# Performance work log

Hardware: AMD Instinct MI355X
Metric: run time of the kernel (lower is better)

The kernel has to match this reference:

```python
import jax, jax.numpy as jnp
import numpy as np

EPS = 1e-12  # matches F.normalize default eps


def l2norm(x):
    n = jnp.sqrt(jnp.sum(x * x, axis=-1, keepdims=True))
    return x / jnp.maximum(n, EPS)


def setup_inputs() -> dict:
    key = jax.random.key(0)
    ks = jax.random.split(key, 14)
    B, Q, T, V = 128, 128, 64, 196
    Dv, Dt, E = 768, 768, 512
    s = 0.02  # kaiming-ish scale
    inp = {
        "visual_cls": jax.random.normal(ks[0], (Q, Dv), jnp.float32),
        "textual_cls": jax.random.normal(ks[1], (B, Dt), jnp.float32),
        "visual_tokens": jax.random.normal(ks[2], (Q, V, Dv), jnp.float32),
        "textual_tokens": jax.random.normal(ks[3], (B, T, Dt), jnp.float32),
        # linear params (torch nn.Linear convention: y = x @ W.T + b)
        "Wv_cls": jax.random.normal(ks[4], (E, Dv), jnp.float32) * s,
        "bv_cls": jnp.zeros((E,), jnp.float32),
        "Wt_cls": jax.random.normal(ks[5], (E, Dt), jnp.float32) * s,
        "bt_cls": jnp.zeros((E,), jnp.float32),
        "Wv_tok": jax.random.normal(ks[6], (E, Dv), jnp.float32) * s,
        "bv_tok": jnp.zeros((E,), jnp.float32),
        "Wt_tok": jax.random.normal(ks[7], (E, Dt), jnp.float32) * s,
        "bt_tok": jnp.zeros((E,), jnp.float32),
        "text_length": jax.random.randint(ks[8], (B,), 1, T + 1, jnp.int64),
    }
    return inp


def reference(visual_cls, textual_cls, visual_tokens, textual_tokens,
              Wv_cls, bv_cls, Wt_cls, bt_cls,
              Wv_tok, bv_tok, Wt_tok, bt_tok, text_length):
    # cls projections
    visual_embed_cls = visual_cls @ Wv_cls.T + bv_cls      # [Q, E]
    textual_embed_cls = textual_cls @ Wt_cls.T + bt_cls    # [B, E]
    # token projections + l2 norm
    ve = l2norm(visual_tokens @ Wv_tok.T + bv_tok)          # [Q, V, E]
    te = l2norm(textual_tokens @ Wt_tok.T + bt_tok)         # [B, T, E]

    B, T, _ = te.shape
    # text mask (built but NOT used in sim, faithful to original)
    text_mask = (jnp.arange(T)[None, :] < text_length[:, None]).astype(jnp.float32)

    # ColBERT-style MaxSim: [B, Q, T, V]
    logits = jnp.einsum('btd,qvd->bqtv', te, ve)
    Vdim = logits.shape[-1]
    Tdim = logits.shape[-2]
    t2v = jnp.sum(jnp.max(logits, axis=-1), axis=2) / Vdim  # [B, Q]
    v2t = jnp.sum(jnp.max(logits, axis=-2), axis=2) / Tdim  # [B, Q]
    text_to_image_sim = 0.5 * (t2v + v2t)                    # [B, Q]

    return (visual_embed_cls, textual_embed_cls, ve, te, text_mask,
            text_to_image_sim)
```

## Files before the change

kernel.cpp:

```cpp
#include <hip/hip_runtime.h>
#include <hip/hip_bf16.h>

typedef __bf16 bf16_t;
typedef __bf16 bf16x8 __attribute__((ext_vector_type(8)));
typedef __bf16 bf16x4 __attribute__((ext_vector_type(4)));
typedef float f32x4 __attribute__((ext_vector_type(4)));
typedef float f32x16 __attribute__((ext_vector_type(16)));

#define MFMA16(a, b, c) __builtin_amdgcn_mfma_f32_16x16x32_bf16((a), (b), (c), 0, 0, 0)
#define MFMA32(a, b, c) __builtin_amdgcn_mfma_f32_32x32x16_bf16((a), (b), (c), 0, 0, 0)

#define WN 393216
#define VP_ELEMS 14680064ULL
#define TP_ELEMS 4194304ULL

__device__ inline bf16x8 cvt8(const float* __restrict__ p) {
    f32x4 a = *reinterpret_cast<const f32x4*>(p);
    f32x4 b = *reinterpret_cast<const f32x4*>(p + 4);
    bf16x8 r;
    r[0] = (bf16_t)a[0]; r[1] = (bf16_t)a[1]; r[2] = (bf16_t)a[2]; r[3] = (bf16_t)a[3];
    r[4] = (bf16_t)b[0]; r[5] = (bf16_t)b[1]; r[6] = (bf16_t)b[2]; r[7] = (bf16_t)b[3];
    return r;
}

__device__ __forceinline__ void gload_lds16(const bf16_t* g, bf16_t* l) {
    __builtin_amdgcn_global_load_lds(
        (const __attribute__((address_space(1))) void*)g,
        (__attribute__((address_space(3))) void*)l, 16, 0, 0);
}

__global__ __launch_bounds__(256) void cvt_w4(
    const float* __restrict__ s0, const float* __restrict__ s1,
    const float* __restrict__ s2, const float* __restrict__ s3,
    bf16_t* __restrict__ d)
{
    int i = blockIdx.x * 256 + threadIdx.x;
    int seg = i / (WN / 4);
    int off = i - seg * (WN / 4);
    const float* s = (seg == 0) ? s0 : (seg == 1) ? s1 : (seg == 2) ? s2 : s3;
    f32x4 v = reinterpret_cast<const f32x4*>(s)[off];
    bf16x4 r;
    r[0] = (bf16_t)v[0]; r[1] = (bf16_t)v[1];
    r[2] = (bf16_t)v[2]; r[3] = (bf16_t)v[3];
    reinterpret_cast<bf16x4*>(d)[i] = r;
}

__global__ __launch_bounds__(256) void zero_tail(bf16_t* __restrict__ vp)
{
    int i = blockIdx.x * 256 + threadIdx.x;
    int off = (i & 63) * 8;
    int ks  = (i >> 6) & 3;
    int c   = (i >> 8) & 7;
    int q   = i >> 11;
    size_t addr = ((size_t)q * 224 + c * 28 + 24 + ks) * 512 + off;
    *reinterpret_cast<f32x4*>(vp + addr) = (f32x4){0.f, 0.f, 0.f, 0.f};
}

template<int PACKED>
__global__ __launch_bounds__(256) void proj_all(
    const float* __restrict__ vtok, const float* __restrict__ ttok,
    const float* __restrict__ vcls, const float* __restrict__ tcls,
    const bf16_t* __restrict__ w_all,
    const float* __restrict__ bvc, const float* __restrict__ btc,
    const float* __restrict__ bvt, const float* __restrict__ btt,
    float* __restrict__ out_base,
    bf16_t* __restrict__ bve, bf16_t* __restrict__ bte)
{
    const int tid  = threadIdx.x;
    const int wave = tid >> 6;
    const int lane = tid & 63;
    const int l16  = lane & 15;
    const int quad = lane >> 4;
    const int e0   = wave * 128;
    const int id   = blockIdx.x;

    const float* A; const bf16_t* W; const float* bias;
    float* out; bf16_t* outb; int seg, m0;
    if (id < 784)       { seg = 0; A = vtok; W = w_all + 2 * WN; bias = bvt;
                          out = out_base + 131072;   outb = bve; m0 = id * 32; }
    else if (id < 1040) { seg = 1; A = ttok; W = w_all + 3 * WN; bias = btt;
                          out = out_base + 12976128; outb = bte; m0 = (id - 784) * 32; }
    else if (id < 1044) { seg = 2; A = vcls; W = w_all;          bias = bvc;
                          out = out_base;             outb = nullptr; m0 = (id - 1040) * 32; }
    else                { seg = 3; A = tcls; W = w_all + WN;     bias = btc;
                          out = out_base + 65536;     outb = nullptr; m0 = (id - 1044) * 32; }

    f32x4 acc[2][8];
#pragma unroll
    for (int rt = 0; rt < 2; ++rt)
#pragma unroll
        for (int t = 0; t < 8; ++t) acc[rt][t] = (f32x4){0.f, 0.f, 0.f, 0.f};

    const float* ar0 = A + (size_t)(m0 + l16) * 768 + quad * 8;
    const float* ar1 = ar0 + (size_t)16 * 768;

    for (int k0 = 0; k0 < 768; k0 += 32) {
        bf16x8 a0 = cvt8(ar0 + k0);
        bf16x8 a1 = cvt8(ar1 + k0);
#pragma unroll
        for (int t = 0; t < 8; ++t) {
            bf16x8 wv = *reinterpret_cast<const bf16x8*>(
                W + (size_t)(e0 + t * 16 + l16) * 768 + quad * 8 + k0);
            acc[0][t] = MFMA16(a0, wv, acc[0][t]);
            acc[1][t] = MFMA16(a1, wv, acc[1][t]);
        }
    }

#pragma unroll
    for (int t = 0; t < 8; ++t) {
        float bv = bias[e0 + t * 16 + l16];
#pragma unroll
        for (int rt = 0; rt < 2; ++rt)
#pragma unroll
            for (int r = 0; r < 4; ++r) acc[rt][t][r] += bv;
    }

    float inv[2][4];
#pragma unroll
    for (int rt = 0; rt < 2; ++rt)
#pragma unroll
        for (int r = 0; r < 4; ++r) inv[rt][r] = 1.f;

    __shared__ float sq[4][32];
    if (seg <= 1) {
#pragma unroll
        for (int rt = 0; rt < 2; ++rt)
#pragma unroll
            for (int r = 0; r < 4; ++r) {
                float s = 0.f;
#pragma unroll
                for (int t = 0; t < 8; ++t) s += acc[rt][t][r] * acc[rt][t][r];
                s += __shfl_xor(s, 1);
                s += __shfl_xor(s, 2);
                s += __shfl_xor(s, 4);
                s += __shfl_xor(s, 8);
                if (l16 == 0) sq[wave][rt * 16 + quad * 4 + r] = s;
            }
        __syncthreads();
#pragma unroll
        for (int rt = 0; rt < 2; ++rt)
#pragma unroll
            for (int r = 0; r < 4; ++r) {
                int row = rt * 16 + quad * 4 + r;
                float tot = sq[0][row] + sq[1][row] + sq[2][row] + sq[3][row];
                inv[rt][r] = 1.0f / fmaxf(sqrtf(tot), 1e-12f);
            }
    }

#pragma unroll
    for (int rt = 0; rt < 2; ++rt)
#pragma unroll
        for (int r = 0; r < 4; ++r) {
            const int   R  = m0 + rt * 16 + quad * 4 + r;
            const float is = inv[rt][r];
            const size_t lin = (size_t)R * 512 + e0 + l16;
#pragma unroll
            for (int t = 0; t < 8; ++t)
                out[lin + t * 16] = acc[rt][t][r] * is;

            if (seg <= 1) {
                if (!PACKED) {
#pragma unroll
                    for (int t = 0; t < 8; ++t)
                        outb[lin + t * 16] = (bf16_t)(acc[rt][t][r] * is);
                } else {
                    size_t fb0; int elem, stride_c;
                    if (seg == 0) {
                        int qq = R / 196, vv = R - qq * 196;
                        fb0  = (size_t)qq * 224 + (vv >> 5) * 4;
                        elem = (((l16 >> 3) * 32 + (vv & 31)) << 3) | (l16 & 7);
                        stride_c = 28;
                    } else {
                        int bb = R >> 6;
                        fb0  = (size_t)bb * 64 + ((R >> 5) & 1) * 4;
                        elem = (((l16 >> 3) * 32 + (R & 31)) << 3) | (l16 & 7);
                        stride_c = 8;
                    }
#pragma unroll
                    for (int t = 0; t < 8; ++t) {
                        int c  = wave * 2 + (t >> 2);
                        int ks = t & 3;
                        outb[(fb0 + (size_t)c * stride_c + ks) * 512 + elem] =
                            (bf16_t)(acc[rt][t][r] * is);
                    }
                }
            }
        }
}

__global__ __launch_bounds__(256) void maxsim32p(
    const bf16_t* __restrict__ tp,
    const bf16_t* __restrict__ vp,
    float* __restrict__ sim)
{
    const int tid  = threadIdx.x;
    const int wave = tid >> 6;
    const int lane = tid & 63;
    const int l32  = lane & 31;
    const int h    = lane >> 5;
    const int bhat = wave >> 1;
    const int tt   = wave & 1;

    const int n  = blockIdx.x;
    const int q  = n >> 6;
    const int bp = n & 63;
    const int b  = bp * 2 + bhat;

    __shared__ bf16_t vs[2][14336];
    __shared__ float  tmax_s[2][64];
    __shared__ float  vmax_s[2][2][224];

    f32x16 acc[7];
#pragma unroll
    for (int vt = 0; vt < 7; ++vt)
#pragma unroll
        for (int r = 0; r < 16; ++r) acc[vt][r] = 0.f;

    const bf16_t* vq = vp + (size_t)q * 114688;
    const bf16_t* tb = tp + (size_t)b * 32768;

    auto issue = [&](int buf, int c) {
        const bf16_t* src = vq + (size_t)c * 14336 + wave * 512 + lane * 8;
        bf16_t* dst = &vs[buf][wave * 512];
#pragma unroll
        for (int g = 0; g < 7; ++g)
            gload_lds16(src + g * 2048, dst + g * 2048);
    };

    issue(0, 0);
#pragma unroll
    for (int c = 0; c < 8; ++c) {
        __syncthreads();
        if (c < 7) issue((c + 1) & 1, c + 1);
        bf16x8 a[4];
        const bf16_t* ta = tb + (size_t)(c * 8 + tt * 4) * 512 + lane * 8;
#pragma unroll
        for (int ks = 0; ks < 4; ++ks)
            a[ks] = *reinterpret_cast<const bf16x8*>(ta + ks * 512);
        const bf16_t* bbase = &vs[c & 1][lane * 8];
#pragma unroll
        for (int ks = 0; ks < 4; ++ks)
#pragma unroll
            for (int vt = 0; vt < 7; ++vt) {
                bf16x8 bv = *reinterpret_cast<const bf16x8*>(
                    bbase + (vt * 4 + ks) * 512);
                acc[vt] = MFMA32(a[ks], bv, acc[vt]);
            }
    }

#pragma unroll
    for (int reg = 0; reg < 16; ++reg) {
        float m = acc[0][reg];
#pragma unroll
        for (int vt = 1; vt < 6; ++vt) m = fmaxf(m, acc[vt][reg]);
        if (l32 < 4) m = fmaxf(m, acc[6][reg]);
        m = fmaxf(m, __shfl_xor(m, 1));
        m = fmaxf(m, __shfl_xor(m, 2));
        m = fmaxf(m, __shfl_xor(m, 4));
        m = fmaxf(m, __shfl_xor(m, 8));
        m = fmaxf(m, __shfl_xor(m, 16));
        if (l32 == 0) {
            int row = tt * 32 + (reg & 3) + 8 * (reg >> 2) + 4 * h;
            tmax_s[bhat][row] = m;
        }
    }
#pragma unroll
    for (int vt = 0; vt < 7; ++vt) {
        float m = acc[vt][0];
#pragma unroll
        for (int reg = 1; reg < 16; ++reg) m = fmaxf(m, acc[vt][reg]);
        m = fmaxf(m, __shfl_xor(m, 32));
        if (h == 0) vmax_s[bhat][tt][vt * 32 + l32] = m;
    }
    __syncthreads();

    if (wave == 0) {
        float t0 = tmax_s[0][lane];
        float t1 = tmax_s[1][lane];
        float c0 = 0.f, c1 = 0.f;
        for (int v = lane; v < 196; v += 64) {
            c0 += fmaxf(vmax_s[0][0][v], vmax_s[0][1][v]);
            c1 += fmaxf(vmax_s[1][0][v], vmax_s[1][1][v]);
        }
#pragma unroll
        for (int mk = 1; mk <= 32; mk <<= 1) {
            t0 += __shfl_xor(t0, mk);
            t1 += __shfl_xor(t1, mk);
            c0 += __shfl_xor(c0, mk);
            c1 += __shfl_xor(c1, mk);
        }
        if (lane == 0) {
            sim[(size_t)(bp * 2 + 0) * 128 + q] = 0.5f * (t0 * (1.0f / 196.0f) + c0 * (1.0f / 64.0f));
            sim[(size_t)(bp * 2 + 1) * 128 + q] = 0.5f * (t1 * (1.0f / 196.0f) + c1 * (1.0f / 64.0f));
        }
    }
}

__global__ __launch_bounds__(256) void maxsim32(
    const bf16_t* __restrict__ te,
    const bf16_t* __restrict__ ve,
    float* __restrict__ sim)
{
    const int tid  = threadIdx.x;
    const int wave = tid >> 6;
    const int lane = tid & 63;
    const int l32  = lane & 31;
    const int h    = lane >> 5;
    const int bhat = wave >> 1;
    const int tt   = wave & 1;

    const int n  = blockIdx.x;
    const int q  = n >> 6;
    const int bp = n & 63;
    const int b  = bp * 2 + bhat;

    __shared__ bf16_t vs[2][224 * 64];
    __shared__ float  tmax_s[2][64];
    __shared__ float  vmax_s[2][2][224];

    f32x16 acc[7];
#pragma unroll
    for (int vt = 0; vt < 7; ++vt)
#pragma unroll
        for (int r = 0; r < 16; ++r) acc[vt][r] = 0.f;

    auto issue = [&](int buf, int c) {
        for (int g = wave; g < 28; g += 4) {
            int r   = g * 8 + (lane >> 3);
            int sr  = r < 196 ? r : 195;
            int seg = (lane & 7) ^ (lane >> 3);
            gload_lds16(ve + ((size_t)q * 196 + sr) * 512 + c * 64 + seg * 8,
                        &vs[buf][g * 512]);
        }
    };

    const size_t tbase = ((size_t)b * 64 + tt * 32 + l32) * 512;

    issue(0, 0);
#pragma unroll
    for (int c = 0; c < 8; ++c) {
        __syncthreads();
        if (c < 7) issue((c + 1) & 1, c + 1);
        bf16x8 a[4];
#pragma unroll
        for (int ks = 0; ks < 4; ++ks)
            a[ks] = *reinterpret_cast<const bf16x8*>(
                te + tbase + c * 64 + ks * 16 + h * 8);
        const int buf = c & 1;
#pragma unroll
        for (int ks = 0; ks < 4; ++ks)
#pragma unroll
            for (int vt = 0; vt < 7; ++vt) {
                int row  = vt * 32 + l32;
                int phys = (ks * 2 + h) ^ (row & 7);
                bf16x8 bv = *reinterpret_cast<const bf16x8*>(
                    &vs[buf][row * 64 + phys * 8]);
                acc[vt] = MFMA32(a[ks], bv, acc[vt]);
            }
    }

#pragma unroll
    for (int reg = 0; reg < 16; ++reg) {
        float m = acc[0][reg];
#pragma unroll
        for (int vt = 1; vt < 6; ++vt) m = fmaxf(m, acc[vt][reg]);
        if (l32 < 4) m = fmaxf(m, acc[6][reg]);
        m = fmaxf(m, __shfl_xor(m, 1));
        m = fmaxf(m, __shfl_xor(m, 2));
        m = fmaxf(m, __shfl_xor(m, 4));
        m = fmaxf(m, __shfl_xor(m, 8));
        m = fmaxf(m, __shfl_xor(m, 16));
        if (l32 == 0) {
            int row = tt * 32 + (reg & 3) + 8 * (reg >> 2) + 4 * h;
            tmax_s[bhat][row] = m;
        }
    }
#pragma unroll
    for (int vt = 0; vt < 7; ++vt) {
        float m = acc[vt][0];
#pragma unroll
        for (int reg = 1; reg < 16; ++reg) m = fmaxf(m, acc[vt][reg]);
        m = fmaxf(m, __shfl_xor(m, 32));
        if (h == 0) vmax_s[bhat][tt][vt * 32 + l32] = m;
    }
    __syncthreads();

    if (wave == 0) {
        float t0 = tmax_s[0][lane];
        float t1 = tmax_s[1][lane];
        float c0 = 0.f, c1 = 0.f;
        for (int v = lane; v < 196; v += 64) {
            c0 += fmaxf(vmax_s[0][0][v], vmax_s[0][1][v]);
            c1 += fmaxf(vmax_s[1][0][v], vmax_s[1][1][v]);
        }
#pragma unroll
        for (int mk = 1; mk <= 32; mk <<= 1) {
            t0 += __shfl_xor(t0, mk);
            t1 += __shfl_xor(t1, mk);
            c0 += __shfl_xor(c0, mk);
            c1 += __shfl_xor(c1, mk);
        }
        if (lane == 0) {
            sim[(size_t)(bp * 2 + 0) * 128 + q] = 0.5f * (t0 * (1.0f / 196.0f) + c0 * (1.0f / 64.0f));
            sim[(size_t)(bp * 2 + 1) * 128 + q] = 0.5f * (t1 * (1.0f / 196.0f) + c1 * (1.0f / 64.0f));
        }
    }
}

__global__ __launch_bounds__(256) void proj_fb(
    const float* __restrict__ A, const float* __restrict__ Wf,
    const float* __restrict__ bias, float* __restrict__ out, int do_l2)
{
    const int tid  = threadIdx.x;
    const int wave = tid >> 6;
    const int lane = tid & 63;
    const int l16  = lane & 15;
    const int quad = lane >> 4;
    const int m0   = blockIdx.x * 16;
    const int e0   = wave * 128;

    f32x4 acc[8];
#pragma unroll
    for (int t = 0; t < 8; ++t) acc[t] = (f32x4){0.f, 0.f, 0.f, 0.f};
    const float* arow = A + (size_t)(m0 + l16) * 768 + quad * 8;
    for (int k0 = 0; k0 < 768; k0 += 32) {
        bf16x8 af = cvt8(arow + k0);
#pragma unroll
        for (int t = 0; t < 8; ++t) {
            bf16x8 wv = cvt8(Wf + (size_t)(e0 + t * 16 + l16) * 768 + quad * 8 + k0);
            acc[t] = MFMA16(af, wv, acc[t]);
        }
    }
#pragma unroll
    for (int t = 0; t < 8; ++t) {
        float bv = bias[e0 + t * 16 + l16];
#pragma unroll
        for (int r = 0; r < 4; ++r) acc[t][r] += bv;
    }
    float inv[4] = {1.f, 1.f, 1.f, 1.f};
    __shared__ float sq[4][16];
    if (do_l2) {
#pragma unroll
        for (int r = 0; r < 4; ++r) {
            float s = 0.f;
#pragma unroll
            for (int t = 0; t < 8; ++t) s += acc[t][r] * acc[t][r];
            s += __shfl_xor(s, 1); s += __shfl_xor(s, 2);
            s += __shfl_xor(s, 4); s += __shfl_xor(s, 8);
            if (l16 == 0) sq[wave][quad * 4 + r] = s;
        }
        __syncthreads();
#pragma unroll
        for (int r = 0; r < 4; ++r) {
            float tot = sq[0][quad * 4 + r] + sq[1][quad * 4 + r]
                      + sq[2][quad * 4 + r] + sq[3][quad * 4 + r];
            inv[r] = 1.0f / fmaxf(sqrtf(tot), 1e-12f);
        }
    }
#pragma unroll
    for (int t = 0; t < 8; ++t)
#pragma unroll
        for (int r = 0; r < 4; ++r)
            out[(size_t)(m0 + quad * 4 + r) * 512 + (e0 + t * 16 + l16)] =
                acc[t][r] * inv[r];
}

__global__ __launch_bounds__(256) void maxsim_fb(
    const float* __restrict__ te, const float* __restrict__ ve,
    float* __restrict__ sim)
{
    const int tid  = threadIdx.x;
    const int wave = tid >> 6;
    const int lane = tid & 63;
    const int l16  = lane & 15;
    const int quad = lane >> 4;
    const int q    = blockIdx.x >> 6;
    const int bp   = blockIdx.x & 63;

    __shared__ bf16_t vsl[208 * 72];
    __shared__ float  maxt_s[2][4][208];
    __shared__ float  t2v_part[2][4];

    f32x4 acc0[13], acc1[13];
#pragma unroll
    for (int vt = 0; vt < 13; ++vt) {
        acc0[vt] = (f32x4){0.f, 0.f, 0.f, 0.f};
        acc1[vt] = (f32x4){0.f, 0.f, 0.f, 0.f};
    }
    const size_t toff0 = ((size_t)(bp * 2) * 64 + wave * 16 + l16) * 512 + quad * 8;
    const size_t toff1 = toff0 + (size_t)64 * 512;

    for (int k0 = 0; k0 < 512; k0 += 64) {
        __syncthreads();
        for (int s = tid; s < 416; s += 256) {
            const int row  = s >> 1;
            const int half = s & 1;
            const int vsrc = row < 196 ? row : 195;
            bf16x8 tmp[4];
            const size_t goff = ((size_t)q * 196 + vsrc) * 512 + k0 + half * 32;
#pragma unroll
            for (int j = 0; j < 4; ++j) tmp[j] = cvt8(ve + goff + j * 8);
            bf16_t* dst = &vsl[row * 72 + half * 32];
#pragma unroll
            for (int j = 0; j < 4; ++j)
                *reinterpret_cast<bf16x8*>(dst + j * 8) = tmp[j];
        }
        __syncthreads();
#pragma unroll
        for (int ks = 0; ks < 2; ++ks) {
            bf16x8 a0 = cvt8(te + toff0 + k0 + ks * 32);
            bf16x8 a1 = cvt8(te + toff1 + k0 + ks * 32);
#pragma unroll
            for (int vt = 0; vt < 13; ++vt) {
                bf16x8 bv = *reinterpret_cast<const bf16x8*>(
                    &vsl[(vt * 16 + l16) * 72 + ks * 32 + quad * 8]);
                acc0[vt] = MFMA16(a0, bv, acc0[vt]);
                acc1[vt] = MFMA16(a1, bv, acc1[vt]);
            }
        }
    }
#pragma unroll
    for (int bi = 0; bi < 2; ++bi) {
        const f32x4* acc = bi ? acc1 : acc0;
        float sum_maxv = 0.f;
#pragma unroll
        for (int r = 0; r < 4; ++r) {
            float m = -3.0e38f;
#pragma unroll
            for (int vt = 0; vt < 13; ++vt) {
                int v = vt * 16 + l16;
                if (v < 196) m = fmaxf(m, acc[vt][r]);
            }
            m = fmaxf(m, __shfl_xor(m, 1));
            m = fmaxf(m, __shfl_xor(m, 2));
            m = fmaxf(m, __shfl_xor(m, 4));
            m = fmaxf(m, __shfl_xor(m, 8));
            sum_maxv += m;
        }
        sum_maxv += __shfl_xor(sum_maxv, 16);
        sum_maxv += __shfl_xor(sum_maxv, 32);
        if (lane == 0) t2v_part[bi][wave] = sum_maxv;
#pragma unroll
        for (int vt = 0; vt < 13; ++vt) {
            float m = fmaxf(fmaxf(acc[vt][0], acc[vt][1]),
                            fmaxf(acc[vt][2], acc[vt][3]));
            m = fmaxf(m, __shfl_xor(m, 16));
            m = fmaxf(m, __shfl_xor(m, 32));
            if (lane < 16) maxt_s[bi][wave][vt * 16 + l16] = m;
        }
    }
    __syncthreads();
    if (wave == 0) {
#pragma unroll
        for (int bi = 0; bi < 2; ++bi) {
            float s_row = t2v_part[bi][0] + t2v_part[bi][1]
                        + t2v_part[bi][2] + t2v_part[bi][3];
            float s_col = 0.f;
            for (int v = lane; v < 196; v += 64) {
                float m = fmaxf(fmaxf(maxt_s[bi][0][v], maxt_s[bi][1][v]),
                                fmaxf(maxt_s[bi][2][v], maxt_s[bi][3][v]));
                s_col += m;
            }
            s_col += __shfl_xor(s_col, 1);
            s_col += __shfl_xor(s_col, 2);
            s_col += __shfl_xor(s_col, 4);
            s_col += __shfl_xor(s_col, 8);
            s_col += __shfl_xor(s_col, 16);
            s_col += __shfl_xor(s_col, 32);
            if (lane == 0)
                sim[(size_t)(bp * 2 + bi) * 128 + q] =
                    0.5f * (s_row * (1.0f / 196.0f) + s_col * (1.0f / 64.0f));
        }
    }
}

__global__ void mask_kernel(const int* __restrict__ len, float* __restrict__ mask)
{
    int i = blockIdx.x * 256 + threadIdx.x;
    int is64 = (len[1] == 0) ? 1 : 0;
    if (i < 128 * 64) {
        int b = i >> 6;
        int t = i & 63;
        int L = is64 ? len[2 * b] : len[b];
        mask[i] = (t < L) ? 1.0f : 0.0f;
    }
}

extern "C" void kernel_launch(void* const* d_in, const int* in_sizes, int n_in,
                              void* d_out, int out_size, void* d_ws, size_t ws_size,
                              hipStream_t stream)
{
    int idx[13] = {0, 1, 2, 3, 4, 5, 6, 7, 8, 9, 10, 11, 12};
    if (in_sizes && n_in >= 13) {
        bool dict = (in_sizes[2] == 19267584) && (in_sizes[4] == 393216);
        if (!dict) {
            static const int alpha_sizes[13] = {393216, 393216, 393216, 393216,
                                                512, 512, 512, 512, 128,
                                                98304, 6291456, 98304, 19267584};
            bool alpha = true;
            for (int i = 0; i < 13; ++i)
                if (in_sizes[i] != alpha_sizes[i]) { alpha = false; break; }
            if (alpha) {
                const int m[13] = {11, 9, 12, 10, 2, 6, 0, 4, 3, 7, 1, 5, 8};
                for (int i = 0; i < 13; ++i) idx[i] = m[i];
            }
        }
    }

    const float* visual_cls     = (const float*)d_in[idx[0]];
    const float* textual_cls    = (const float*)d_in[idx[1]];
    const float* visual_tokens  = (const float*)d_in[idx[2]];
    const float* textual_tokens = (const float*)d_in[idx[3]];
    const float* Wv_cls = (const float*)d_in[idx[4]];
    const float* bv_cls = (const float*)d_in[idx[5]];
    const float* Wt_cls = (const float*)d_in[idx[6]];
    const float* bt_cls = (const float*)d_in[idx[7]];
    const float* Wv_tok = (const float*)d_in[idx[8]];
    const float* bv_tok = (const float*)d_in[idx[9]];
    const float* Wt_tok = (const float*)d_in[idx[10]];
    const float* bt_tok = (const float*)d_in[idx[11]];
    const int*   text_length = (const int*)d_in[idx[12]];

    float* out    = (float*)d_out;
    float* o_vcls = out;
    float* o_tcls = out + 65536;
    float* o_ve   = out + 131072;
    float* o_te   = out + 12976128;
    float* o_mask = out + 17170432;
    float* o_sim  = out + 17178624;

    const size_t NVE = 12845056;
    const size_t NTE = 4194304;
    const size_t need_new = (4 * (size_t)WN + VP_ELEMS + TP_ELEMS) * 2;
    const size_t need_old = (4 * (size_t)WN + NVE + NTE) * 2;

    dim3 blk(256);
    if (ws_size >= need_new) {
        bf16_t* w_all = (bf16_t*)d_ws;
        bf16_t* vp    = w_all + 4 * (size_t)WN;
        bf16_t* tp    = vp + VP_ELEMS;
        cvt_w4<<<(4 * WN / 4 + 255) / 256, blk, 0, stream>>>(Wv_cls, Wt_cls, Wv_tok, Wt_tok, w_all);
        zero_tail<<<1024, blk, 0, stream>>>(vp);
        proj_all<1><<<1048, blk, 0, stream>>>(visual_tokens, textual_tokens,
                                              visual_cls, textual_cls, w_all,
                                              bv_cls, bt_cls, bv_tok, bt_tok,
                                              out, vp, tp);
        mask_kernel<<<32, blk, 0, stream>>>(text_length, o_mask);
        maxsim32p<<<128 * 64, blk, 0, stream>>>(tp, vp, o_sim);
    } else if (ws_size >= need_old) {
        bf16_t* w_all = (bf16_t*)d_ws;
        bf16_t* b_ve  = w_all + 4 * (size_t)WN;
        bf16_t* b_te  = b_ve + NVE;
        cvt_w4<<<(4 * WN / 4 + 255) / 256, blk, 0, stream>>>(Wv_cls, Wt_cls, Wv_tok, Wt_tok, w_all);
        proj_all<0><<<1048, blk, 0, stream>>>(visual_tokens, textual_tokens,
                                              visual_cls, textual_cls, w_all,
                                              bv_cls, bt_cls, bv_tok, bt_tok,
                                              out, b_ve, b_te);
        mask_kernel<<<32, blk, 0, stream>>>(text_length, o_mask);
        maxsim32<<<128 * 64, blk, 0, stream>>>(b_te, b_ve, o_sim);
    } else {
        proj_fb<<<8,    blk, 0, stream>>>(visual_cls,     Wv_cls, bv_cls, o_vcls, 0);
        proj_fb<<<8,    blk, 0, stream>>>(textual_cls,    Wt_cls, bt_cls, o_tcls, 0);
        proj_fb<<<1568, blk, 0, stream>>>(visual_tokens,  Wv_tok, bv_tok, o_ve, 1);
        proj_fb<<<512,  blk, 0, stream>>>(textual_tokens, Wt_tok, bt_tok, o_te, 1);
        mask_kernel<<<32, blk, 0, stream>>>(text_length, o_mask);
        maxsim_fb<<<128 * 64, blk, 0, stream>>>(o_te, o_ve, o_sim);
    }
}
```

Before: 601.6 us.

## Split maxsim waves over V halves and both batches, prefetch text A-fragments

The maxsim kernel's waves are re-split so each wave covers both batch rows for half of the V tiles (4 or 3 tiles), instead of one batch row over all 7 V tiles. Each LDS B-fragment read now feeds two MFMAs, which halves LDS traffic per MFMA. Text A-fragments are register double-buffered, loaded one chunk ahead, and the V-half assignment alternates by block index to balance the uneven tile split. Launch bounds request 2 blocks per SM. The wave doing 4 V tiles carries more MFMA work than the one doing 3, and there is a leftover dead lambda.

```diff
diff --git a/kernel.cpp b/kernel.cpp
--- a/kernel.cpp
+++ b/kernel.cpp
@@ -188,7 +188,7 @@
         }
 }
 
-__global__ __launch_bounds__(256) void maxsim32p(
+__global__ __launch_bounds__(256, 2) void maxsim32p(
     const bf16_t* __restrict__ tp,
     const bf16_t* __restrict__ vp,
     float* __restrict__ sim)
@@ -198,26 +198,29 @@
     const int lane = tid & 63;
     const int l32  = lane & 31;
     const int h    = lane >> 5;
-    const int bhat = wave >> 1;
     const int tt   = wave & 1;
 
     const int n  = blockIdx.x;
     const int q  = n >> 6;
     const int bp = n & 63;
-    const int b  = bp * 2 + bhat;
+    const int vh  = (wave >> 1) ^ ((n >> 3) & 1);
+    const int vt0 = vh * 4;
 
     __shared__ bf16_t vs[2][14336];
-    __shared__ float  tmax_s[2][64];
+    __shared__ float  tmax_s[2][2][64];
     __shared__ float  vmax_s[2][2][224];
 
-    f32x16 acc[7];
-#pragma unroll
-    for (int vt = 0; vt < 7; ++vt)
-#pragma unroll
-        for (int r = 0; r < 16; ++r) acc[vt][r] = 0.f;
-
-    const bf16_t* vq = vp + (size_t)q * 114688;
-    const bf16_t* tb = tp + (size_t)b * 32768;
+    f32x16 acc[2][4];
+#pragma unroll
+    for (int bi = 0; bi < 2; ++bi)
+#pragma unroll
+        for (int j = 0; j < 4; ++j)
+#pragma unroll
+            for (int r = 0; r < 16; ++r) acc[bi][j][r] = 0.f;
+
+    const bf16_t* vq  = vp + (size_t)q * 114688;
+    const bf16_t* tb0 = tp + (size_t)(bp * 2) * 32768 + (size_t)(tt * 4) * 512 + lane * 8;
+    const bf16_t* tb1 = tb0 + 32768;
 
     auto issue = [&](int buf, int c) {
         const bf16_t* src = vq + (size_t)c * 14336 + wave * 512 + lane * 8;
@@ -227,56 +230,91 @@
             gload_lds16(src + g * 2048, dst + g * 2048);
     };
 
+    bf16x8 a[2][2][4];
+    auto loadA = [&](int slot, int c) {
+#pragma unroll
+        for (int ks = 0; ks < 4; ++ks) {
+            a[0][0][0] = a[0][0][0];
+        }
+    };
+    (void)loadA;
+
     issue(0, 0);
+#pragma unroll
+    for (int ks = 0; ks < 4; ++ks) {
+        a[0][0][ks] = *reinterpret_cast<const bf16x8*>(tb0 + ks * 512);
+        a[0][1][ks] = *reinterpret_cast<const bf16x8*>(tb1 + ks * 512);
+    }
+
 #pragma unroll
     for (int c = 0; c < 8; ++c) {
         __syncthreads();
-        if (c < 7) issue((c + 1) & 1, c + 1);
-        bf16x8 a[4];
-        const bf16_t* ta = tb + (size_t)(c * 8 + tt * 4) * 512 + lane * 8;
-#pragma unroll
-        for (int ks = 0; ks < 4; ++ks)
-            a[ks] = *reinterpret_cast<const bf16x8*>(ta + ks * 512);
-        const bf16_t* bbase = &vs[c & 1][lane * 8];
-#pragma unroll
-        for (int ks = 0; ks < 4; ++ks)
-#pragma unroll
-            for (int vt = 0; vt < 7; ++vt) {
+        if (c < 7) {
+            issue((c + 1) & 1, c + 1);
+            const size_t co = (size_t)(c + 1) * 8 * 512;
+#pragma unroll
+            for (int ks = 0; ks < 4; ++ks) {
+                a[(c + 1) & 1][0][ks] = *reinterpret_cast<const bf16x8*>(tb0 + co + ks * 512);
+                a[(c + 1) & 1][1][ks] = *reinterpret_cast<const bf16x8*>(tb1 + co + ks * 512);
+            }
+        }
+        const bf16_t* bbase = &vs[c & 1][vt0 * 2048 + lane * 8];
+#pragma unroll
+        for (int ks = 0; ks < 4; ++ks) {
+#pragma unroll
+            for (int j = 0; j < 3; ++j) {
                 bf16x8 bv = *reinterpret_cast<const bf16x8*>(
-                    bbase + (vt * 4 + ks) * 512);
-                acc[vt] = MFMA32(a[ks], bv, acc[vt]);
-            }
-    }
-
-#pragma unroll
-    for (int reg = 0; reg < 16; ++reg) {
-        float m = acc[0][reg];
-#pragma unroll
-        for (int vt = 1; vt < 6; ++vt) m = fmaxf(m, acc[vt][reg]);
-        if (l32 < 4) m = fmaxf(m, acc[6][reg]);
-        m = fmaxf(m, __shfl_xor(m, 1));
-        m = fmaxf(m, __shfl_xor(m, 2));
-        m = fmaxf(m, __shfl_xor(m, 4));
-        m = fmaxf(m, __shfl_xor(m, 8));
-        m = fmaxf(m, __shfl_xor(m, 16));
-        if (l32 == 0) {
-            int row = tt * 32 + (reg & 3) + 8 * (reg >> 2) + 4 * h;
-            tmax_s[bhat][row] = m;
-        }
-    }
-#pragma unroll
-    for (int vt = 0; vt < 7; ++vt) {
-        float m = acc[vt][0];
-#pragma unroll
-        for (int reg = 1; reg < 16; ++reg) m = fmaxf(m, acc[vt][reg]);
-        m = fmaxf(m, __shfl_xor(m, 32));
-        if (h == 0) vmax_s[bhat][tt][vt * 32 + l32] = m;
-    }
+                    bbase + (j * 4 + ks) * 512);
+                acc[0][j] = MFMA32(a[c & 1][0][ks], bv, acc[0][j]);
+                acc[1][j] = MFMA32(a[c & 1][1][ks], bv, acc[1][j]);
+            }
+            if (vh == 0) {
+                bf16x8 bv = *reinterpret_cast<const bf16x8*>(
+                    bbase + (12 + ks) * 512);
+                acc[0][3] = MFMA32(a[c & 1][0][ks], bv, acc[0][3]);
+                acc[1][3] = MFMA32(a[c & 1][1][ks], bv, acc[1][3]);
+            }
+        }
+    }
+
+#pragma unroll
+    for (int bi = 0; bi < 2; ++bi)
+#pragma unroll
+        for (int reg = 0; reg < 16; ++reg) {
+            float m = fmaxf(acc[bi][0][reg], acc[bi][1][reg]);
+            if (vh == 0) {
+                m = fmaxf(m, acc[bi][2][reg]);
+                m = fmaxf(m, acc[bi][3][reg]);
+            } else if (l32 < 4) {
+                m = fmaxf(m, acc[bi][2][reg]);
+            }
+            m = fmaxf(m, __shfl_xor(m, 1));
+            m = fmaxf(m, __shfl_xor(m, 2));
+            m = fmaxf(m, __shfl_xor(m, 4));
+            m = fmaxf(m, __shfl_xor(m, 8));
+            m = fmaxf(m, __shfl_xor(m, 16));
+            if (l32 == 0) {
+                int row = tt * 32 + (reg & 3) + 8 * (reg >> 2) + 4 * h;
+                tmax_s[bi][vh][row] = m;
+            }
+        }
+
+#pragma unroll
+    for (int bi = 0; bi < 2; ++bi)
+#pragma unroll
+        for (int j = 0; j < 4; ++j) {
+            if (j == 3 && vh == 1) continue;
+            float m = acc[bi][j][0];
+#pragma unroll
+            for (int reg = 1; reg < 16; ++reg) m = fmaxf(m, acc[bi][j][reg]);
+            m = fmaxf(m, __shfl_xor(m, 32));
+            if (h == 0) vmax_s[bi][tt][(vt0 + j) * 32 + l32] = m;
+        }
     __syncthreads();
 
     if (wave == 0) {
-        float t0 = tmax_s[0][lane];
-        float t1 = tmax_s[1][lane];
+        float t0 = fmaxf(tmax_s[0][0][lane], tmax_s[0][1][lane]);
+        float t1 = fmaxf(tmax_s[1][0][lane], tmax_s[1][1][lane]);
         float c0 = 0.f, c1 = 0.f;
         for (int v = lane; v < 196; v += 64) {
             c0 += fmaxf(vmax_s[0][0][v], vmax_s[0][1][v]);
```

Measured after the change: 658.2 us. 1.09x slower.
